# Optimization experiments

Measured on AMD Instinct MI355X. Metric: run time of the kernel, lower is better.

The kernel has to match this reference:

```python
import jax, jax.numpy as jnp
import numpy as np

N_HEADS = 16
KEY_DIM = 64
VAL_DIM = 64
KV_CH = 512


def setup_inputs() -> dict:
    key = jax.random.key(0)
    k1, k2, k3, k4, k5, k6 = jax.random.split(key, 6)
    B, H, W = 32, 64, 64
    kv = jax.random.normal(k1, (B, H, W, KV_CH), dtype=jnp.float32)
    # 1x1 conv kernels are just [C_in, C_out] matrices
    scale = 1.0 / np.sqrt(KV_CH)
    W_k = jax.random.normal(k2, (KV_CH, N_HEADS * KEY_DIM), dtype=jnp.float32) * scale
    b_k = jnp.zeros((N_HEADS * KEY_DIM,), dtype=jnp.float32)
    W_v = jax.random.normal(k3, (KV_CH, N_HEADS * VAL_DIM), dtype=jnp.float32) * scale
    b_v = jnp.zeros((N_HEADS * VAL_DIM,), dtype=jnp.float32)
    query = jax.random.normal(k4, (1, 1, N_HEADS, KEY_DIM), dtype=jnp.float32) * 0.05
    return {"key_value": kv, "W_k": W_k, "b_k": b_k, "W_v": W_v, "b_v": b_v, "query": query}


def reference(key_value, W_k, b_k, W_v, b_v, query):
    B, H, W, _ = key_value.shape
    HW = H * W
    x = key_value.reshape(B, HW, KV_CH)  # 1x1 conv == per-pixel matmul
    key = (jnp.einsum('bsc,cd->bsd', x, W_k) + b_k).reshape(B, HW, N_HEADS, KEY_DIM)
    value = jnp.tanh(jnp.einsum('bsc,cd->bsd', x, W_v) + b_v).reshape(B, HW, N_HEADS, VAL_DIM)
    # query broadcast dot over key dim -> [B, HW, N]
    dot = jnp.einsum('bsnk,nk->bsn', key, query[0, 0])
    attn = jax.nn.softmax(dot, axis=1)  # softmax over spatial axis
    # inference mode: dropout is identity
    out = jnp.einsum('bsn,bsnv->bnv', attn, value)  # [B, N, V]
    return out
```

## Files before the change

kernel.cpp:

```cpp
#include <hip/hip_runtime.h>
#include <cstdint>

using short8 = __attribute__((ext_vector_type(8))) short;
using f32x4  = __attribute__((ext_vector_type(4))) float;

__device__ __forceinline__ unsigned short bf16rne(float f) {
  unsigned int u = __float_as_uint(f);
  unsigned int r = u + 0x7fffu + ((u >> 16) & 1u);
  return (unsigned short)(r >> 16);
}

__device__ __forceinline__ void gl2lds16(const void* g, void* s) {
  auto gp = reinterpret_cast<const __attribute__((address_space(1))) unsigned int*>(
      reinterpret_cast<uintptr_t>(g));
  auto sp = reinterpret_cast<__attribute__((address_space(3))) unsigned int*>(
      (uint32_t)reinterpret_cast<uintptr_t>(s));
  __builtin_amdgcn_global_load_lds(gp, sp, 16, 0, 0);
}

__device__ __forceinline__ float fast_tanh(float x) {
  float e = __expf(2.0f * x);
  return 1.0f - 2.0f / (e + 1.0f);
}

#define DSR(dst, addr) \
  asm volatile("ds_read_b128 %0, %1" : "=v"(dst) : "v"(addr))

__global__ __launch_bounds__(256) void prep_kernel(
    const float* __restrict__ Wk, const float* __restrict__ q,
    const float* __restrict__ Wv,
    unsigned short* __restrict__ wqb, unsigned short* __restrict__ wvt) {
  __shared__ float T[64 * 65];
  int bid = blockIdx.x;
  if (bid < 32) {
    int idx = bid * 256 + threadIdx.x;
    int n = idx >> 9, c = idx & 511;
    const float* wrow = Wk + (long)c * 1024 + n * 64;
    const float* qrow = q + n * 64;
    float s = 0.f;
    #pragma unroll 8
    for (int k = 0; k < 64; ++k) s += wrow[k] * qrow[k];
    wqb[n * 512 + c] = bf16rne(s);
  } else {
    int t = bid - 32;
    int tc = t & 7, tl = t >> 3;
    int c0 = tc * 64, l0 = tl * 64;
    int j = threadIdx.x & 63, i0 = threadIdx.x >> 6;
    #pragma unroll
    for (int ii = 0; ii < 16; ++ii) {
      int i = i0 * 16 + ii;
      T[i * 65 + j] = Wv[(long)(c0 + i) * 1024 + l0 + j];
    }
    __syncthreads();
    #pragma unroll
    for (int ii = 0; ii < 16; ++ii) {
      int jj = i0 * 16 + ii;
      wvt[(long)(l0 + jj) * 512 + c0 + j] = bf16rne(T[j * 65 + jj]);
    }
  }
}

__global__ __launch_bounds__(256) void dot_kernel(
    const float* __restrict__ kv, const unsigned short* __restrict__ wqb,
    unsigned short* __restrict__ xb, float* __restrict__ dotbuf) {
  __shared__ __align__(16) float AsF[2][128 * 64];
  __shared__ __align__(16) unsigned short Ws[16 * 512];
  int tid = threadIdx.x, l = tid & 63, w = tid >> 6;
  long row0 = (long)blockIdx.x * 128;
  int qd = l >> 4, lm = l & 15;

  for (int j = 0; j < 4; ++j) {
    int n = w * 4 + j;
    gl2lds16(wqb + n * 512 + ((l ^ (n & 7)) * 8), &Ws[n * 512]);
  }

  auto dmaA = [&](int it, int buf) {
    #pragma unroll
    for (int j = 0; j < 8; ++j) {
      int g = (w * 8 + j) * 64 + l;
      int r = g >> 4, c = g & 15;
      int cc = c ^ (r & 14);
      gl2lds16(kv + (row0 + r) * 512 + it * 64 + cc * 4, &AsF[buf][(w * 8 + j) * 256]);
    }
  };

  f32x4 acc[2];
  acc[0] = f32x4{0.f, 0.f, 0.f, 0.f};
  acc[1] = f32x4{0.f, 0.f, 0.f, 0.f};

  dmaA(0, 0);
  for (int it = 0; it < 8; ++it) {
    __syncthreads();
    if (it < 7) dmaA(it + 1, (it + 1) & 1);
    const float* base = &AsF[it & 1][0];
    #pragma unroll
    for (int mi = 0; mi < 2; ++mi) {
      int m = w * 32 + mi * 16 + lm;
      int s = m & 14;
      #pragma unroll
      for (int k32 = 0; k32 < 2; ++k32) {
        int fc = k32 * 8 + qd * 2;
        float4 fa = *(const float4*)&base[(m * 16 + (fc ^ s)) * 4];
        float4 fb = *(const float4*)&base[(m * 16 + ((fc + 1) ^ s)) * 4];
        short8 h;
        h[0] = bf16rne(fa.x); h[1] = bf16rne(fa.y); h[2] = bf16rne(fa.z); h[3] = bf16rne(fa.w);
        h[4] = bf16rne(fb.x); h[5] = bf16rne(fb.y); h[6] = bf16rne(fb.z); h[7] = bf16rne(fb.w);
        *(short8*)&xb[(row0 + m) * 512 + it * 64 + k32 * 32 + qd * 8] = h;
        int cl = it * 8 + k32 * 4 + qd;
        short8 bfrag = *(const short8*)&Ws[lm * 512 + ((cl ^ (lm & 7)) * 8)];
        acc[mi] = __builtin_amdgcn_mfma_f32_16x16x32_bf16(h, bfrag, acc[mi], 0, 0, 0);
      }
    }
  }
  #pragma unroll
  for (int mi = 0; mi < 2; ++mi) {
    long rg = row0 + w * 32 + mi * 16 + qd * 4;
    long b = rg >> 12;
    long s = rg & 4095;
    *(f32x4*)&dotbuf[((b * 16 + lm) << 12) + s] = acc[mi];
  }
}

__global__ __launch_bounds__(256) void softmax_kernel(float* __restrict__ dotbuf) {
  long bn = blockIdx.x;
  float4* p = (float4*)(dotbuf + bn * 4096);
  int tid = threadIdx.x;
  int l = tid & 63, w = tid >> 6;
  float4 v[4];
  float mx = -1e30f;
  #pragma unroll
  for (int i = 0; i < 4; ++i) {
    v[i] = p[tid + i * 256];
    mx = fmaxf(mx, fmaxf(fmaxf(v[i].x, v[i].y), fmaxf(v[i].z, v[i].w)));
  }
  for (int o = 32; o; o >>= 1) mx = fmaxf(mx, __shfl_xor(mx, o, 64));
  __shared__ float redm[4];
  __shared__ float reds[4];
  if (l == 0) redm[w] = mx;
  __syncthreads();
  mx = fmaxf(fmaxf(redm[0], redm[1]), fmaxf(redm[2], redm[3]));
  float s = 0.f;
  #pragma unroll
  for (int i = 0; i < 4; ++i) {
    v[i].x = __expf(v[i].x - mx); v[i].y = __expf(v[i].y - mx);
    v[i].z = __expf(v[i].z - mx); v[i].w = __expf(v[i].w - mx);
    s += v[i].x + v[i].y + v[i].z + v[i].w;
  }
  for (int o = 32; o; o >>= 1) s += __shfl_xor(s, o, 64);
  if (l == 0) reds[w] = s;
  __syncthreads();
  s = reds[0] + reds[1] + reds[2] + reds[3];
  float inv = 1.0f / s;
  #pragma unroll
  for (int i = 0; i < 4; ++i) {
    v[i].x *= inv; v[i].y *= inv; v[i].z *= inv; v[i].w *= inv;
    p[tid + i * 256] = v[i];
  }
}

__global__ __launch_bounds__(512, 2) void out_gemm_kernel(
    const unsigned short* __restrict__ xb, const unsigned short* __restrict__ wvt,
    const float* __restrict__ wn, const float* __restrict__ bv,
    float* __restrict__ out) {
  __shared__ __align__(16) unsigned short As[2][2][8192];
  __shared__ __align__(16) unsigned short Bs[2][2][8192];
  __shared__ float wlds[1024];

  int tid = threadIdx.x, l = tid & 63, w = tid >> 6;
  int qd = l >> 4, lm = l & 15;
  int wm = w >> 2, wnx = w & 3;

  int id = blockIdx.x;
  int ct = (id >> 3) & 3;
  int g  = (id & 7) | ((id >> 5) << 3);
  long row0 = (long)g * 256;
  long b = g >> 4;
  const unsigned short* Ag = xb + row0 * 512;
  const unsigned short* Bg = wvt + (long)ct * 256 * 512;
  int head = ct * 4 + wnx;

  {
    float w0 = wn[((b * 16 + ct * 4 + (tid >> 8)) << 12) + (row0 & 4095) + (tid & 255)];
    int i1 = tid + 512;
    float w1 = wn[((b * 16 + ct * 4 + (i1 >> 8)) << 12) + (row0 & 4095) + (i1 & 255)];
    wlds[tid] = w0;
    wlds[i1] = w1;
  }

  const unsigned short *pa0, *pa1, *pb0, *pb1;
  {
    int pl0 = (w * 2 + 0) * 64 + l;
    int r20 = pl0 >> 3, sub0 = (pl0 & 7) ^ (r20 & 7);
    int ro0 = (r20 * 2 + (sub0 >> 2)) * 512 + (sub0 & 3) * 8;
    pa0 = Ag + ro0;  pb0 = Bg + ro0;
    int pl1 = (w * 2 + 1) * 64 + l;
    int r21 = pl1 >> 3, sub1 = (pl1 & 7) ^ (r21 & 7);
    int ro1 = (r21 * 2 + (sub1 >> 2)) * 512 + (sub1 & 3) * 8;
    pa1 = Ag + ro1;  pb1 = Bg + ro1;
  }
  int d0 = (w * 2 + 0) * 512, d1 = (w * 2 + 1) * 512;

  unsigned asB = (unsigned)(uintptr_t)&As[0][0][0];
  unsigned bsB = (unsigned)(uintptr_t)&Bs[0][0][0];
  unsigned aA[8], bA[4];
  #pragma unroll
  for (int mi = 0; mi < 8; ++mi) {
    int m = wm * 128 + mi * 16 + lm;
    int gi = (m >> 1) * 8 + (((((m & 1) << 2) | qd)) ^ ((m >> 1) & 7));
    aA[mi] = asB + gi * 16;
  }
  #pragma unroll
  for (int ni = 0; ni < 4; ++ni) {
    int n = wnx * 64 + ni * 16 + lm;
    int gi = (n >> 1) * 8 + (((((n & 1) << 2) | qd)) ^ ((n >> 1) & 7));
    bA[ni] = bsB + gi * 16;
  }

  f32x4 acc[8][4];
  #pragma unroll
  for (int mi = 0; mi < 8; ++mi)
    #pragma unroll
    for (int ni = 0; ni < 4; ++ni) acc[mi][ni] = f32x4{0.f, 0.f, 0.f, 0.f};

  gl2lds16(pa0,      &As[0][0][d0]); gl2lds16(pa1,      &As[0][0][d1]);
  gl2lds16(pb0,      &Bs[0][0][d0]); gl2lds16(pb1,      &Bs[0][0][d1]);
  gl2lds16(pa0 + 32, &As[0][1][d0]); gl2lds16(pa1 + 32, &As[0][1][d1]);
  gl2lds16(pb0 + 32, &Bs[0][1][d0]); gl2lds16(pb1 + 32, &Bs[0][1][d1]);
  asm volatile("s_waitcnt vmcnt(4)" ::: "memory");
  asm volatile("s_barrier" ::: "memory");

  #pragma unroll
  for (int t = 0; t < 8; ++t) {
    const int slot = t & 1, ds = slot ^ 1;
    const unsigned sb = (unsigned)slot * 32768;
    const int so = (t + 1) * 64;

    short8 bf0[4], af[4];
    DSR(bf0[0], bA[0] + sb); DSR(bf0[1], bA[1] + sb);
    DSR(bf0[2], bA[2] + sb); DSR(bf0[3], bA[3] + sb);
    DSR(af[0], aA[0] + sb); DSR(af[1], aA[1] + sb);
    DSR(af[2], aA[2] + sb); DSR(af[3], aA[3] + sb);
    if (t < 7) {
      gl2lds16(pa0 + so, &As[ds][0][d0]);
      gl2lds16(pa1 + so, &As[ds][0][d1]);
    }
    asm volatile("s_barrier" ::: "memory");
    asm volatile("s_waitcnt lgkmcnt(0)" ::: "memory");
    __builtin_amdgcn_sched_barrier(0);
    __builtin_amdgcn_s_setprio(1);
    #pragma unroll
    for (int mi = 0; mi < 4; ++mi)
      #pragma unroll
      for (int ni = 0; ni < 4; ++ni)
        acc[mi][ni] = __builtin_amdgcn_mfma_f32_16x16x32_bf16(af[mi], bf0[ni], acc[mi][ni], 0, 0, 0);
    __builtin_amdgcn_s_setprio(0);
    __builtin_amdgcn_sched_barrier(0);
    asm volatile("s_barrier" ::: "memory");

    DSR(af[0], aA[4] + sb); DSR(af[1], aA[5] + sb);
    DSR(af[2], aA[6] + sb); DSR(af[3], aA[7] + sb);
    if (t < 7) {
      gl2lds16(pb0 + so, &Bs[ds][0][d0]);
      gl2lds16(pb1 + so, &Bs[ds][0][d1]);
      asm volatile("s_waitcnt vmcnt(4)" ::: "memory");
    } else {
      asm volatile("s_waitcnt vmcnt(0)" ::: "memory");
    }
    asm volatile("s_barrier" ::: "memory");
    asm volatile("s_waitcnt lgkmcnt(0)" ::: "memory");
    __builtin_amdgcn_sched_barrier(0);
    __builtin_amdgcn_s_setprio(1);
    #pragma unroll
    for (int mi = 0; mi < 4; ++mi)
      #pragma unroll
      for (int ni = 0; ni < 4; ++ni)
        acc[mi + 4][ni] = __builtin_amdgcn_mfma_f32_16x16x32_bf16(af[mi], bf0[ni], acc[mi + 4][ni], 0, 0, 0);
    __builtin_amdgcn_s_setprio(0);
    __builtin_amdgcn_sched_barrier(0);
    asm volatile("s_barrier" ::: "memory");

    short8 bf1[4];
    DSR(bf1[0], bA[0] + sb + 16384); DSR(bf1[1], bA[1] + sb + 16384);
    DSR(bf1[2], bA[2] + sb + 16384); DSR(bf1[3], bA[3] + sb + 16384);
    DSR(af[0], aA[0] + sb + 16384); DSR(af[1], aA[1] + sb + 16384);
    DSR(af[2], aA[2] + sb + 16384); DSR(af[3], aA[3] + sb + 16384);
    if (t < 7) {
      gl2lds16(pa0 + so + 32, &As[ds][1][d0]);
      gl2lds16(pa1 + so + 32, &As[ds][1][d1]);
    }
    asm volatile("s_barrier" ::: "memory");
    asm volatile("s_waitcnt lgkmcnt(0)" ::: "memory");
    __builtin_amdgcn_sched_barrier(0);
    __builtin_amdgcn_s_setprio(1);
    #pragma unroll
    for (int mi = 0; mi < 4; ++mi)
      #pragma unroll
      for (int ni = 0; ni < 4; ++ni)
        acc[mi][ni] = __builtin_amdgcn_mfma_f32_16x16x32_bf16(af[mi], bf1[ni], acc[mi][ni], 0, 0, 0);
    __builtin_amdgcn_s_setprio(0);
    __builtin_amdgcn_sched_barrier(0);
    asm volatile("s_barrier" ::: "memory");

    DSR(af[0], aA[4] + sb + 16384); DSR(af[1], aA[5] + sb + 16384);
    DSR(af[2], aA[6] + sb + 16384); DSR(af[3], aA[7] + sb + 16384);
    if (t < 7) {
      gl2lds16(pb0 + so + 32, &Bs[ds][1][d0]);
      gl2lds16(pb1 + so + 32, &Bs[ds][1][d1]);
      asm volatile("s_waitcnt vmcnt(4)" ::: "memory");
    }
    asm volatile("s_barrier" ::: "memory");
    asm volatile("s_waitcnt lgkmcnt(0)" ::: "memory");
    __builtin_amdgcn_sched_barrier(0);
    __builtin_amdgcn_s_setprio(1);
    #pragma unroll
    for (int mi = 0; mi < 4; ++mi)
      #pragma unroll
      for (int ni = 0; ni < 4; ++ni)
        acc[mi + 4][ni] = __builtin_amdgcn_mfma_f32_16x16x32_bf16(af[mi], bf1[ni], acc[mi + 4][ni], 0, 0, 0);
    __builtin_amdgcn_s_setprio(0);
    __builtin_amdgcn_sched_barrier(0);
    asm volatile("s_barrier" ::: "memory");
  }

  __syncthreads();

  float bias[4];
  #pragma unroll
  for (int ni = 0; ni < 4; ++ni) bias[ni] = bv[head * 64 + ni * 16 + lm];
  float res[4] = {0.f, 0.f, 0.f, 0.f};
  #pragma unroll
  for (int mi = 0; mi < 8; ++mi) {
    int rb = wm * 128 + mi * 16 + qd * 4;
    float w0 = wlds[wnx * 256 + rb + 0];
    float w1 = wlds[wnx * 256 + rb + 1];
    float w2 = wlds[wnx * 256 + rb + 2];
    float w3 = wlds[wnx * 256 + rb + 3];
    #pragma unroll
    for (int ni = 0; ni < 4; ++ni) {
      f32x4 c = acc[mi][ni];
      res[ni] += w0 * fast_tanh(c[0] + bias[ni]) + w1 * fast_tanh(c[1] + bias[ni])
               + w2 * fast_tanh(c[2] + bias[ni]) + w3 * fast_tanh(c[3] + bias[ni]);
    }
  }
  #pragma unroll
  for (int ni = 0; ni < 4; ++ni) {
    float v = res[ni];
    v += __shfl_xor(v, 16, 64);
    v += __shfl_xor(v, 32, 64);
    if (qd == 0)
      atomicAdd(&out[b * 1024 + head * 64 + ni * 16 + lm], v);
  }
}

extern "C" void kernel_launch(void* const* d_in, const int* in_sizes, int n_in,
                              void* d_out, int out_size, void* d_ws, size_t ws_size,
                              hipStream_t stream) {
  const float* kv = (const float*)d_in[0];
  const float* Wk = (const float*)d_in[1];
  const float* Wv = (const float*)d_in[3];
  const float* bv = (const float*)d_in[4];
  const float* q  = (const float*)d_in[5];
  float* out = (float*)d_out;

  char* ws = (char*)d_ws;
  unsigned short* xb  = (unsigned short*)(ws);
  unsigned short* wqb = (unsigned short*)(ws + 134217728);
  unsigned short* wvt = (unsigned short*)(ws + 134217728 + 16384);
  float* dotbuf = (float*)(ws + 134217728 + 16384 + 1048576);

  hipMemsetAsync(d_out, 0, 32768 * sizeof(float), stream);
  prep_kernel<<<160, 256, 0, stream>>>(Wk, q, Wv, wqb, wvt);
  dot_kernel<<<1024, 256, 0, stream>>>(kv, wqb, xb, dotbuf);
  softmax_kernel<<<512, 256, 0, stream>>>(dotbuf);
  out_gemm_kernel<<<2048, 512, 0, stream>>>(xb, wvt, dotbuf, bv, out);
}
```

Before: 584.0 us.

## Load B operand directly from global into registers and cut per-stage barriers

Drops the LDS staging buffer for the weight (B) operand of the output GEMM. Each lane now loads its MFMA B fragments straight from global memory into double-buffered registers. The A-tile prefetch for a whole k-step is issued at once, so only two barriers per iteration remain instead of eight. This aims to cut LDS traffic, LDS footprint and synchronisation. In exchange it raises register pressure (16 extra short8 registers at 512 threads, 2 blocks) and has each wave fetch B from global/L2 redundantly.

```diff
diff --git a/kernel.cpp b/kernel.cpp
--- a/kernel.cpp
+++ b/kernel.cpp
@@ -25,6 +25,11 @@
 
 #define DSR(dst, addr) \
   asm volatile("ds_read_b128 %0, %1" : "=v"(dst) : "v"(addr))
+#define GLB(dst, p) \
+  asm volatile("global_load_dwordx4 %0, %1, off" : "=v"(dst) : "v"(p))
+#define GLB64(dst, p) \
+  asm volatile("global_load_dwordx4 %0, %1, off offset:64" : "=v"(dst) : "v"(p))
+#define KEEP(x) asm volatile("" : "+v"(x))
 
 __global__ __launch_bounds__(256) void prep_kernel(
     const float* __restrict__ Wk, const float* __restrict__ q,
@@ -163,7 +168,6 @@
     const float* __restrict__ wn, const float* __restrict__ bv,
     float* __restrict__ out) {
   __shared__ __align__(16) unsigned short As[2][2][8192];
-  __shared__ __align__(16) unsigned short Bs[2][2][8192];
   __shared__ float wlds[1024];
 
   int tid = threadIdx.x, l = tid & 63, w = tid >> 6;
@@ -187,34 +191,30 @@
     wlds[i1] = w1;
   }
 
-  const unsigned short *pa0, *pa1, *pb0, *pb1;
+  const unsigned short *pa0, *pa1;
   {
     int pl0 = (w * 2 + 0) * 64 + l;
     int r20 = pl0 >> 3, sub0 = (pl0 & 7) ^ (r20 & 7);
-    int ro0 = (r20 * 2 + (sub0 >> 2)) * 512 + (sub0 & 3) * 8;
-    pa0 = Ag + ro0;  pb0 = Bg + ro0;
+    pa0 = Ag + (r20 * 2 + (sub0 >> 2)) * 512 + (sub0 & 3) * 8;
     int pl1 = (w * 2 + 1) * 64 + l;
     int r21 = pl1 >> 3, sub1 = (pl1 & 7) ^ (r21 & 7);
-    int ro1 = (r21 * 2 + (sub1 >> 2)) * 512 + (sub1 & 3) * 8;
-    pa1 = Ag + ro1;  pb1 = Bg + ro1;
+    pa1 = Ag + (r21 * 2 + (sub1 >> 2)) * 512 + (sub1 & 3) * 8;
   }
   int d0 = (w * 2 + 0) * 512, d1 = (w * 2 + 1) * 512;
 
   unsigned asB = (unsigned)(uintptr_t)&As[0][0][0];
-  unsigned bsB = (unsigned)(uintptr_t)&Bs[0][0][0];
-  unsigned aA[8], bA[4];
+  unsigned aA[8];
   #pragma unroll
   for (int mi = 0; mi < 8; ++mi) {
     int m = wm * 128 + mi * 16 + lm;
     int gi = (m >> 1) * 8 + (((((m & 1) << 2) | qd)) ^ ((m >> 1) & 7));
     aA[mi] = asB + gi * 16;
   }
-  #pragma unroll
-  for (int ni = 0; ni < 4; ++ni) {
-    int n = wnx * 64 + ni * 16 + lm;
-    int gi = (n >> 1) * 8 + (((((n & 1) << 2) | qd)) ^ ((n >> 1) & 7));
-    bA[ni] = bsB + gi * 16;
-  }
+
+  const unsigned short* pB[4];
+  #pragma unroll
+  for (int ni = 0; ni < 4; ++ni)
+    pB[ni] = Bg + (wnx * 64 + ni * 16 + lm) * 512 + qd * 8;
 
   f32x4 acc[8][4];
   #pragma unroll
@@ -222,29 +222,45 @@
     #pragma unroll
     for (int ni = 0; ni < 4; ++ni) acc[mi][ni] = f32x4{0.f, 0.f, 0.f, 0.f};
 
+  short8 bfr[2][8];
+
   gl2lds16(pa0,      &As[0][0][d0]); gl2lds16(pa1,      &As[0][0][d1]);
-  gl2lds16(pb0,      &Bs[0][0][d0]); gl2lds16(pb1,      &Bs[0][0][d1]);
   gl2lds16(pa0 + 32, &As[0][1][d0]); gl2lds16(pa1 + 32, &As[0][1][d1]);
-  gl2lds16(pb0 + 32, &Bs[0][1][d0]); gl2lds16(pb1 + 32, &Bs[0][1][d1]);
-  asm volatile("s_waitcnt vmcnt(4)" ::: "memory");
-  asm volatile("s_barrier" ::: "memory");
+  GLB  (bfr[0][0], pB[0]); GLB64(bfr[0][1], pB[0]);
+  GLB  (bfr[0][2], pB[1]); GLB64(bfr[0][3], pB[1]);
+  GLB  (bfr[0][4], pB[2]); GLB64(bfr[0][5], pB[2]);
+  GLB  (bfr[0][6], pB[3]); GLB64(bfr[0][7], pB[3]);
+  pB[0] += 64; pB[1] += 64; pB[2] += 64; pB[3] += 64;
 
   #pragma unroll
   for (int t = 0; t < 8; ++t) {
     const int slot = t & 1, ds = slot ^ 1;
     const unsigned sb = (unsigned)slot * 32768;
-    const int so = (t + 1) * 64;
-
-    short8 bf0[4], af[4];
-    DSR(bf0[0], bA[0] + sb); DSR(bf0[1], bA[1] + sb);
-    DSR(bf0[2], bA[2] + sb); DSR(bf0[3], bA[3] + sb);
+
+    asm volatile("s_barrier" ::: "memory");
+    if (t < 7) {
+      const int so = (t + 1) * 64;
+      gl2lds16(pa0 + so,      &As[ds][0][d0]);
+      gl2lds16(pa1 + so,      &As[ds][0][d1]);
+      gl2lds16(pa0 + so + 32, &As[ds][1][d0]);
+      gl2lds16(pa1 + so + 32, &As[ds][1][d1]);
+      GLB  (bfr[ds][0], pB[0]); GLB64(bfr[ds][1], pB[0]);
+      GLB  (bfr[ds][2], pB[1]); GLB64(bfr[ds][3], pB[1]);
+      GLB  (bfr[ds][4], pB[2]); GLB64(bfr[ds][5], pB[2]);
+      GLB  (bfr[ds][6], pB[3]); GLB64(bfr[ds][7], pB[3]);
+      pB[0] += 64; pB[1] += 64; pB[2] += 64; pB[3] += 64;
+      asm volatile("s_waitcnt vmcnt(12)" ::: "memory");
+    } else {
+      asm volatile("s_waitcnt vmcnt(0)" ::: "memory");
+    }
+    asm volatile("s_barrier" ::: "memory");
+
+    KEEP(bfr[slot][0]); KEEP(bfr[slot][1]); KEEP(bfr[slot][2]); KEEP(bfr[slot][3]);
+    KEEP(bfr[slot][4]); KEEP(bfr[slot][5]); KEEP(bfr[slot][6]); KEEP(bfr[slot][7]);
+
+    short8 af[4];
     DSR(af[0], aA[0] + sb); DSR(af[1], aA[1] + sb);
     DSR(af[2], aA[2] + sb); DSR(af[3], aA[3] + sb);
-    if (t < 7) {
-      gl2lds16(pa0 + so, &As[ds][0][d0]);
-      gl2lds16(pa1 + so, &As[ds][0][d1]);
-    }
-    asm volatile("s_barrier" ::: "memory");
     asm volatile("s_waitcnt lgkmcnt(0)" ::: "memory");
     __builtin_amdgcn_sched_barrier(0);
     __builtin_amdgcn_s_setprio(1);
@@ -252,21 +268,11 @@
     for (int mi = 0; mi < 4; ++mi)
       #pragma unroll
       for (int ni = 0; ni < 4; ++ni)
-        acc[mi][ni] = __builtin_amdgcn_mfma_f32_16x16x32_bf16(af[mi], bf0[ni], acc[mi][ni], 0, 0, 0);
+        acc[mi][ni] = __builtin_amdgcn_mfma_f32_16x16x32_bf16(af[mi], bfr[slot][ni * 2], acc[mi][ni], 0, 0, 0);
     __builtin_amdgcn_s_setprio(0);
     __builtin_amdgcn_sched_barrier(0);
-    asm volatile("s_barrier" ::: "memory");
-
     DSR(af[0], aA[4] + sb); DSR(af[1], aA[5] + sb);
     DSR(af[2], aA[6] + sb); DSR(af[3], aA[7] + sb);
-    if (t < 7) {
-      gl2lds16(pb0 + so, &Bs[ds][0][d0]);
-      gl2lds16(pb1 + so, &Bs[ds][0][d1]);
-      asm volatile("s_waitcnt vmcnt(4)" ::: "memory");
-    } else {
-      asm volatile("s_waitcnt vmcnt(0)" ::: "memory");
-    }
-    asm volatile("s_barrier" ::: "memory");
     asm volatile("s_waitcnt lgkmcnt(0)" ::: "memory");
     __builtin_amdgcn_sched_barrier(0);
     __builtin_amdgcn_s_setprio(1);
@@ -274,21 +280,11 @@
     for (int mi = 0; mi < 4; ++mi)
       #pragma unroll
       for (int ni = 0; ni < 4; ++ni)
-        acc[mi + 4][ni] = __builtin_amdgcn_mfma_f32_16x16x32_bf16(af[mi], bf0[ni], acc[mi + 4][ni], 0, 0, 0);
+        acc[mi + 4][ni] = __builtin_amdgcn_mfma_f32_16x16x32_bf16(af[mi], bfr[slot][ni * 2], acc[mi + 4][ni], 0, 0, 0);
     __builtin_amdgcn_s_setprio(0);
     __builtin_amdgcn_sched_barrier(0);
-    asm volatile("s_barrier" ::: "memory");
-
-    short8 bf1[4];
-    DSR(bf1[0], bA[0] + sb + 16384); DSR(bf1[1], bA[1] + sb + 16384);
-    DSR(bf1[2], bA[2] + sb + 16384); DSR(bf1[3], bA[3] + sb + 16384);
     DSR(af[0], aA[0] + sb + 16384); DSR(af[1], aA[1] + sb + 16384);
     DSR(af[2], aA[2] + sb + 16384); DSR(af[3], aA[3] + sb + 16384);
-    if (t < 7) {
-      gl2lds16(pa0 + so + 32, &As[ds][1][d0]);
-      gl2lds16(pa1 + so + 32, &As[ds][1][d1]);
-    }
-    asm volatile("s_barrier" ::: "memory");
     asm volatile("s_waitcnt lgkmcnt(0)" ::: "memory");
     __builtin_amdgcn_sched_barrier(0);
     __builtin_amdgcn_s_setprio(1);
@@ -296,19 +292,11 @@
     for (int mi = 0; mi < 4; ++mi)
       #pragma unroll
       for (int ni = 0; ni < 4; ++ni)
-        acc[mi][ni] = __builtin_amdgcn_mfma_f32_16x16x32_bf16(af[mi], bf1[ni], acc[mi][ni], 0, 0, 0);
+        acc[mi][ni] = __builtin_amdgcn_mfma_f32_16x16x32_bf16(af[mi], bfr[slot][ni * 2 + 1], acc[mi][ni], 0, 0, 0);
     __builtin_amdgcn_s_setprio(0);
     __builtin_amdgcn_sched_barrier(0);
-    asm volatile("s_barrier" ::: "memory");
-
     DSR(af[0], aA[4] + sb + 16384); DSR(af[1], aA[5] + sb + 16384);
     DSR(af[2], aA[6] + sb + 16384); DSR(af[3], aA[7] + sb + 16384);
-    if (t < 7) {
-      gl2lds16(pb0 + so + 32, &Bs[ds][1][d0]);
-      gl2lds16(pb1 + so + 32, &Bs[ds][1][d1]);
-      asm volatile("s_waitcnt vmcnt(4)" ::: "memory");
-    }
-    asm volatile("s_barrier" ::: "memory");
     asm volatile("s_waitcnt lgkmcnt(0)" ::: "memory");
     __builtin_amdgcn_sched_barrier(0);
     __builtin_amdgcn_s_setprio(1);
@@ -316,10 +304,9 @@
     for (int mi = 0; mi < 4; ++mi)
       #pragma unroll
       for (int ni = 0; ni < 4; ++ni)
-        acc[mi + 4][ni] = __builtin_amdgcn_mfma_f32_16x16x32_bf16(af[mi], bf1[ni], acc[mi + 4][ni], 0, 0, 0);
+        acc[mi + 4][ni] = __builtin_amdgcn_mfma_f32_16x16x32_bf16(af[mi], bfr[slot][ni * 2 + 1], acc[mi + 4][ni], 0, 0, 0);
     __builtin_amdgcn_s_setprio(0);
     __builtin_amdgcn_sched_barrier(0);
-    asm volatile("s_barrier" ::: "memory");
   }
 
   __syncthreads();
```

Measured after the change: 662.9 us. 1.14x slower.
